# Optimization experiments

Hardware: AMD Instinct MI355X
Metric: run time of the kernel (lower is better)

The kernel has to match this reference:

```python
import jax, jax.numpy as jnp
import numpy as np

LN_EPS = 1e-5

def _ln(x, g, b):
    m = jnp.mean(x, -1, keepdims=True)
    v = jnp.mean((x - m) ** 2, -1, keepdims=True)
    return (x - m) / jnp.sqrt(v + LN_EPS) * g + b

def setup_inputs() -> dict:
    key = jax.random.key(0)
    N, E, D, F = 200000, 6400000, 128, 2048
    ks = iter(jax.random.split(key, 32))
    def rn(shape, sc):
        return jax.random.normal(next(ks), shape, jnp.float32) * sc
    inp = dict(
        x=rn((N, 3), 1.0),
        edge_index=jax.random.randint(next(ks), (2, E), 0, N),
        Win=rn((D, 3), 0.5), b_in=rn((D,), 0.02),
        Wv=rn((3, D, D), 0.08), bv=rn((3, D), 0.02),
        Wo=rn((3, D, D), 0.08), bo=rn((3, D), 0.02),
        W1=rn((3, F, D), 0.08), b1=rn((3, F), 0.02),
        W2=rn((3, D, F), 0.02), b2=rn((3, D), 0.02),
        ln1g=jnp.ones((3, D), jnp.float32), ln1b=jnp.zeros((3, D), jnp.float32),
        ln2g=jnp.ones((3, D), jnp.float32), ln2b=jnp.zeros((3, D), jnp.float32),
        Wd=rn((1, D), 0.08), bd=rn((1,), 0.02),
        Wg=rn((32, 1), 0.5), bg=rn((32,), 0.02),
        Wf=rn((1, 32), 0.2), bf=rn((1,), 0.02),
    )
    return inp

def reference(x, edge_index, Win, b_in, Wv, bv, Wo, bo, W1, b1, W2, b2,
              ln1g, ln1b, ln2g, ln2b, Wd, bd, Wg, bg, Wf, bf):
    N = x.shape[0]
    h = jax.nn.relu(x @ Win.T + b_in)  # [N, 128]
    # TransformerEncoder with seq_len == 1: softmax over a single key is 1,
    # so self-attention output == out_proj(value_proj(h)); post-norm layers.
    for i in range(3):
        attn = (h @ Wv[i].T + bv[i]) @ Wo[i].T + bo[i]
        h = _ln(h + attn, ln1g[i], ln1b[i])
        ff = jax.nn.relu(h @ W1[i].T + b1[i]) @ W2[i].T + b2[i]  # [N, 2048] intermediate
        h = _ln(h + ff, ln2g[i], ln2b[i])
    z = jax.nn.relu(h @ Wd.T + bd)  # [N, 1]
    # GCNConv(1, 32): add self-loops, symmetric D^-1/2 (A+I) D^-1/2 normalization
    self_idx = jnp.arange(N)
    row = jnp.concatenate([edge_index[0], self_idx])  # source
    col = jnp.concatenate([edge_index[1], self_idx])  # target
    xw = z @ Wg.T  # [N, 32]
    deg = jax.ops.segment_sum(jnp.ones_like(col, jnp.float32), col, num_segments=N)
    dis = jax.lax.rsqrt(jnp.maximum(deg, 1.0))
    norm = dis[row] * dis[col]  # [E + N]
    agg = jax.ops.segment_sum(xw[row] * norm[:, None], col, num_segments=N) + bg
    zr = jax.nn.relu(agg)  # [N, 32]
    return zr @ Wf.T + bf  # [N, 1]
```

## Files before the change

### kernel.cpp

```cpp
#include <hip/hip_runtime.h>
#include <hip/hip_bf16.h>
#include <stdint.h>

typedef __attribute__((ext_vector_type(8))) short short8;
typedef __attribute__((ext_vector_type(4))) float f32x4;

#define LN_EPS 1e-5f

__device__ __forceinline__ ushort f2bf(float f) {
  union { float f; uint32_t u; } v; v.f = f;
  uint32_t u = v.u;
  return (ushort)((u + 0x7FFFu + ((u >> 16) & 1u)) >> 16);
}
__device__ __forceinline__ float bf2f(ushort b) {
  union { uint32_t u; float f; } v; v.u = ((uint32_t)b) << 16;
  return v.f;
}
__device__ __forceinline__ uint32_t cvtpk(float lo, float hi) {
  uint32_t r;
  asm volatile("v_cvt_pk_bf16_f32 %0, %1, %2" : "=v"(r) : "v"(lo), "v"(hi));
  return r;
}


__global__ void conv_bf16_kernel(const float* __restrict__ src, ushort* __restrict__ dst, int n) {
  int i = blockIdx.x * 256 + threadIdx.x;
  if (i < n) dst[i] = f2bf(src[i]);
}

__global__ void zero_kernel(float* __restrict__ p, int n) {
  int i = blockIdx.x * 256 + threadIdx.x;
  if (i < n) p[i] = 0.f;
}

__global__ void embed_kernel(const float* __restrict__ x, const float* __restrict__ Win,
                             const float* __restrict__ b_in, float* __restrict__ h, int N) {
  int i = blockIdx.x * 256 + threadIdx.x;
  if (i >= N * 128) return;
  int n = i >> 7, d = i & 127;
  float v = Win[d*3+0]*x[n*3+0] + Win[d*3+1]*x[n*3+1] + Win[d*3+2]*x[n*3+2] + b_in[d];
  h[i] = fmaxf(v, 0.f);
}

__global__ void deg_kernel(const int* __restrict__ ei, float* __restrict__ degf, int E) {
  int i = blockIdx.x * 256 + threadIdx.x;
  int e0 = i * 4;
  if (e0 + 3 < E) {
    int4 c = *(const int4*)(ei + E + e0);
    atomicAdd(&degf[c.x], 1.0f); atomicAdd(&degf[c.y], 1.0f);
    atomicAdd(&degf[c.z], 1.0f); atomicAdd(&degf[c.w], 1.0f);
  } else {
    for (int e = e0; e < E; ++e) atomicAdd(&degf[ei[E + e]], 1.0f);
  }
}

__global__ void z_kernel(const float* __restrict__ h, const float* __restrict__ wd,
                         const float* __restrict__ bd, const float* __restrict__ degf,
                         float* __restrict__ u, int N) {
  int row = blockIdx.x * 4 + (threadIdx.x >> 6);
  int lane = threadIdx.x & 63;
  if (row >= N) return;
  const float* hr = h + (size_t)row * 128;
  float s = hr[lane] * wd[lane] + hr[64 + lane] * wd[64 + lane];
  #pragma unroll
  for (int o = 32; o >= 1; o >>= 1) s += __shfl_xor(s, o, 64);
  if (lane == 0) {
    float z = fmaxf(s + bd[0], 0.f);
    u[row] = z * rsqrtf(degf[row] + 1.0f);
  }
}

__global__ void scatter_kernel(const int* __restrict__ ei, const float* __restrict__ u,
                               float* __restrict__ t, int E) {
  int i = blockIdx.x * 256 + threadIdx.x;
  int e0 = i * 4;
  if (e0 + 3 < E) {
    int4 r = *(const int4*)(ei + e0);
    int4 c = *(const int4*)(ei + E + e0);
    atomicAdd(&t[c.x], u[r.x]); atomicAdd(&t[c.y], u[r.y]);
    atomicAdd(&t[c.z], u[r.z]); atomicAdd(&t[c.w], u[r.w]);
  } else {
    for (int e = e0; e < E; ++e) atomicAdd(&t[ei[E + e]], u[ei[e]]);
  }
}

__global__ void out_kernel(const float* __restrict__ degf, const float* __restrict__ u,
                           const float* __restrict__ t, const float* __restrict__ wg,
                           const float* __restrict__ bg, const float* __restrict__ wf,
                           const float* __restrict__ bfp, float* __restrict__ out, int N) {
  int n = blockIdx.x * 256 + threadIdx.x;
  if (n >= N) return;
  float dis = rsqrtf(degf[n] + 1.0f);
  float tf = dis * (t[n] + u[n]);
  float acc = bfp[0];
  #pragma unroll
  for (int j = 0; j < 32; ++j) acc += wf[j] * fmaxf(tf * wg[j] + bg[j], 0.f);
  out[n] = acc;
}


#define MFMA16(a, b, c) __builtin_amdgcn_mfma_f32_16x16x32_bf16(a, b, c, 0, 0, 0)

__global__ __launch_bounds__(512, 2) void layer_kernel(
    float* __restrict__ h,
    const ushort* __restrict__ Wv, const ushort* __restrict__ Wo,
    const ushort* __restrict__ W1, const ushort* __restrict__ W2,
    const float* __restrict__ bv, const float* __restrict__ bo,
    const float* __restrict__ b1, const float* __restrict__ b2,
    const float* __restrict__ g1, const float* __restrict__ be1,
    const float* __restrict__ g2, const float* __restrict__ be2,
    int N)
{
  __shared__ ushort hA[256 * 128];
  __shared__ ushort wbuf[2 * 16384];

  const int tid = threadIdx.x;
  const int lane = tid & 63;
  const int wave = tid >> 6;
  const int l15 = lane & 15;
  const int lg = lane >> 4;
  const int rowbase = blockIdx.x * 256;
  const int wrow = wave * 32;
  const int ssw = (l15 & 7) << 4;

  #pragma unroll
  for (int i = 0; i < 8; ++i) {
    int u = tid + i * 512;
    int row = u >> 4, k8 = u & 15;
    int g = rowbase + row;
    float4 f0 = make_float4(0.f,0.f,0.f,0.f), f1 = f0;
    if (g < N) {
      const float4* p = (const float4*)(h + (size_t)g * 128 + k8 * 8);
      f0 = p[0]; f1 = p[1];
    }
    short8 v;
    v[0]=(short)f2bf(f0.x); v[1]=(short)f2bf(f0.y); v[2]=(short)f2bf(f0.z); v[3]=(short)f2bf(f0.w);
    v[4]=(short)f2bf(f1.x); v[5]=(short)f2bf(f1.y); v[6]=(short)f2bf(f1.z); v[7]=(short)f2bf(f1.w);
    *(short8*)((char*)hA + ((row << 8) + ((k8 << 4) ^ ((row & 7) << 4)))) = v;
  }
  #pragma unroll
  for (int i = 0; i < 4; ++i) {
    int u = tid + i * 512;
    int row = u >> 4, k8 = u & 15;
    int off = (row << 8) + ((k8 << 4) ^ ((row & 7) << 4));
    *(short8*)((char*)wbuf + off)         = *(const short8*)(Wv + u * 8);
    *(short8*)((char*)wbuf + 32768 + off) = *(const short8*)(Wo + u * 8);
  }
  __syncthreads();

  short8 wr[4];
  #pragma unroll
  for (int i = 0; i < 4; ++i) {
    int c = tid + i * 512;
    wr[i] = (c < 1024) ? *(const short8*)(W1 + c * 8)
                       : *(const short8*)(W2 + (size_t)((c - 1024) >> 3) * 2048 + ((c - 1024) & 7) * 8);
  }

  f32x4 tC[2][8];
  #pragma unroll
  for (int rt = 0; rt < 2; ++rt)
    #pragma unroll
    for (int ct = 0; ct < 8; ++ct) tC[rt][ct] = (f32x4){0.f,0.f,0.f,0.f};
  __builtin_amdgcn_s_setprio(1);
  #pragma unroll
  for (int ks = 0; ks < 4; ++ks) {
    int asw = (ks * 64 + lg * 16) ^ ssw;
    short8 a0 = *(const short8*)((char*)hA + (((wrow + l15) << 8) + asw));
    short8 a1 = *(const short8*)((char*)hA + (((wrow + 16 + l15) << 8) + asw));
    #pragma unroll
    for (int ct = 0; ct < 8; ++ct) {
      short8 b = *(const short8*)((char*)wbuf + (((ct * 16 + l15) << 8) + asw));
      tC[0][ct] = MFMA16(a0, b, tC[0][ct]);
      tC[1][ct] = MFMA16(a1, b, tC[1][ct]);
    }
  }
  __builtin_amdgcn_s_setprio(0);
  #pragma unroll
  for (int ct = 0; ct < 8; ++ct) {
    int col = ct * 16 + l15;
    float bvv = bv[col];
    #pragma unroll
    for (int rt = 0; rt < 2; ++rt)
      #pragma unroll
      for (int j = 0; j < 4; ++j) {
        int lr = wrow + rt * 16 + lg * 4 + j;
        *(ushort*)((char*)hA + ((lr << 8) + ((col * 2) ^ ((lr & 7) << 4)))) =
            f2bf(tC[rt][ct][j] + bvv);
      }
  }
  __syncthreads();

  #pragma unroll
  for (int rt = 0; rt < 2; ++rt)
    #pragma unroll
    for (int ct = 0; ct < 8; ++ct) tC[rt][ct] = (f32x4){0.f,0.f,0.f,0.f};
  __builtin_amdgcn_s_setprio(1);
  #pragma unroll
  for (int ks = 0; ks < 4; ++ks) {
    int asw = (ks * 64 + lg * 16) ^ ssw;
    short8 a0 = *(const short8*)((char*)hA + (((wrow + l15) << 8) + asw));
    short8 a1 = *(const short8*)((char*)hA + (((wrow + 16 + l15) << 8) + asw));
    #pragma unroll
    for (int ct = 0; ct < 8; ++ct) {
      short8 b = *(const short8*)((char*)wbuf + 32768 + (((ct * 16 + l15) << 8) + asw));
      tC[0][ct] = MFMA16(a0, b, tC[0][ct]);
      tC[1][ct] = MFMA16(a1, b, tC[1][ct]);
    }
  }
  __builtin_amdgcn_s_setprio(0);

  float sum[2][4] = {{0,0,0,0},{0,0,0,0}};
  float sq[2][4]  = {{0,0,0,0},{0,0,0,0}};
  #pragma unroll
  for (int rt = 0; rt < 2; ++rt)
    #pragma unroll
    for (int ct = 0; ct < 8; ++ct) {
      float bov = bo[ct * 16 + l15];
      #pragma unroll
      for (int j = 0; j < 4; ++j) {
        int g = rowbase + wrow + rt * 16 + lg * 4 + j;
        float hv = (g < N) ? h[(size_t)g * 128 + ct * 16 + l15] : 0.f;
        float v = tC[rt][ct][j] + bov + hv;
        tC[rt][ct][j] = v;
        sum[rt][j] += v; sq[rt][j] += v * v;
      }
    }
  #pragma unroll
  for (int o = 1; o < 16; o <<= 1)
    #pragma unroll
    for (int rt = 0; rt < 2; ++rt)
      #pragma unroll
      for (int j = 0; j < 4; ++j) {
        sum[rt][j] += __shfl_xor(sum[rt][j], o, 64);
        sq[rt][j]  += __shfl_xor(sq[rt][j],  o, 64);
      }
  float mean[2][4], rstd[2][4];
  #pragma unroll
  for (int rt = 0; rt < 2; ++rt)
    #pragma unroll
    for (int j = 0; j < 4; ++j) {
      mean[rt][j] = sum[rt][j] * (1.f / 128.f);
      float var = sq[rt][j] * (1.f / 128.f) - mean[rt][j] * mean[rt][j];
      rstd[rt][j] = rsqrtf(var + LN_EPS);
    }
  #pragma unroll
  for (int ct = 0; ct < 8; ++ct) {
    int col = ct * 16 + l15;
    float g1v = g1[col], b1v = be1[col];
    #pragma unroll
    for (int rt = 0; rt < 2; ++rt)
      #pragma unroll
      for (int j = 0; j < 4; ++j) {
        int lr = wrow + rt * 16 + lg * 4 + j;
        float hh = (tC[rt][ct][j] - mean[rt][j]) * rstd[rt][j] * g1v + b1v;
        *(ushort*)((char*)hA + ((lr << 8) + ((col * 2) ^ ((lr & 7) << 4)))) = f2bf(hh);
      }
  }

  #pragma unroll
  for (int i = 0; i < 4; ++i) {
    int c = tid + i * 512;
    if (c < 1024) {
      int row = c >> 4, k8 = c & 15;
      *(short8*)((char*)wbuf + ((row << 8) + ((k8 << 4) ^ ((row & 7) << 4)))) = wr[i];
    } else {
      int cc = c - 1024;
      int row = cc >> 3, k8 = cc & 7;
      *(short8*)((char*)wbuf + 16384 + ((row << 7) + ((k8 << 4) ^ ((row & 7) << 4)))) = wr[i];
    }
  }
  {
    const ushort* W1c = W1 + 64 * 128;
    const ushort* W2c = W2 + 64;
    #pragma unroll
    for (int i = 0; i < 4; ++i) {
      int c = tid + i * 512;
      wr[i] = (c < 1024) ? *(const short8*)(W1c + c * 8)
                         : *(const short8*)(W2c + (size_t)((c - 1024) >> 3) * 2048 + ((c - 1024) & 7) * 8);
    }
  }
  __syncthreads();

  f32x4 acc[2][8];
  #pragma unroll
  for (int rt = 0; rt < 2; ++rt)
    #pragma unroll
    for (int ct = 0; ct < 8; ++ct) acc[rt][ct] = (f32x4){0.f,0.f,0.f,0.f};

  for (int ch = 0; ch < 32; ++ch) {
    const int base = (ch & 1) << 15;
    f32x4 uT[4][2];
    #pragma unroll
    for (int ft = 0; ft < 4; ++ft)
      #pragma unroll
      for (int rt = 0; rt < 2; ++rt) uT[ft][rt] = (f32x4){0.f,0.f,0.f,0.f};
    __builtin_amdgcn_s_setprio(1);
    #pragma unroll
    for (int ks = 0; ks < 4; ++ks) {
      int asw = (ks * 64 + lg * 16) ^ ssw;
      short8 bh[2];
      #pragma unroll
      for (int rt = 0; rt < 2; ++rt)
        bh[rt] = *(const short8*)((char*)hA + (((wrow + rt * 16 + l15) << 8) + asw));
      #pragma unroll
      for (int ft = 0; ft < 4; ++ft) {
        short8 aw = *(const short8*)((char*)wbuf + base + (((ft * 16 + l15) << 8) + asw));
        uT[ft][0] = MFMA16(aw, bh[0], uT[ft][0]);
        uT[ft][1] = MFMA16(aw, bh[1], uT[ft][1]);
      }
    }
    __builtin_amdgcn_s_setprio(0);
    #pragma unroll
    for (int ft = 0; ft < 4; ++ft) {
      float4 b4 = *(const float4*)(b1 + ch * 64 + ft * 16 + lg * 4);
      #pragma unroll
      for (int rt = 0; rt < 2; ++rt)
        #pragma unroll
        for (int j = 0; j < 4; ++j)
          uT[ft][rt][j] = fmaxf(uT[ft][rt][j] + ((const float*)&b4)[j], 0.f);
    }
    short8 fr[2][2];
    {
      const int s0 = l15 + ((lg & 1) << 5);
      const int s1 = s0 + 16;
      const bool hiq = (lg >= 2);
      #pragma unroll
      for (int ks2 = 0; ks2 < 2; ++ks2)
        #pragma unroll
        for (int rt = 0; rt < 2; ++rt) {
          uint32_t pA0 = cvtpk(uT[2*ks2][rt][0],   uT[2*ks2][rt][1]);
          uint32_t pA1 = cvtpk(uT[2*ks2][rt][2],   uT[2*ks2][rt][3]);
          uint32_t pB0 = cvtpk(uT[2*ks2+1][rt][0], uT[2*ks2+1][rt][1]);
          uint32_t pB1 = cvtpk(uT[2*ks2+1][rt][2], uT[2*ks2+1][rt][3]);
          uint32_t d0 = __shfl((int)pA0, s0, 64), d1 = __shfl((int)pA1, s0, 64);
          uint32_t d2 = __shfl((int)pA0, s1, 64), d3 = __shfl((int)pA1, s1, 64);
          uint32_t e0 = __shfl((int)pB0, s0, 64), e1 = __shfl((int)pB1, s0, 64);
          uint32_t e2 = __shfl((int)pB0, s1, 64), e3 = __shfl((int)pB1, s1, 64);
          union { uint32_t u[4]; short8 s; } f;
          f.u[0] = hiq ? e0 : d0; f.u[1] = hiq ? e1 : d1;
          f.u[2] = hiq ? e2 : d2; f.u[3] = hiq ? e3 : d3;
          fr[rt][ks2] = f.s;
        }
    }
    __builtin_amdgcn_s_setprio(1);
    #pragma unroll
    for (int ks2 = 0; ks2 < 2; ++ks2) {
      int asw2 = (ks2 * 64 + lg * 16) ^ ssw;
      #pragma unroll
      for (int ct = 0; ct < 8; ++ct) {
        short8 b = *(const short8*)((char*)wbuf + base + 16384 + (((ct * 16 + l15) << 7) + asw2));
        acc[0][ct] = MFMA16(fr[0][ks2], b, acc[0][ct]);
        acc[1][ct] = MFMA16(fr[1][ks2], b, acc[1][ct]);
      }
    }
    __builtin_amdgcn_s_setprio(0);

    if (ch < 31) {
      const int nbase = ((ch + 1) & 1) << 15;
      #pragma unroll
      for (int i = 0; i < 4; ++i) {
        int c = tid + i * 512;
        if (c < 1024) {
          int row = c >> 4, k8 = c & 15;
          *(short8*)((char*)wbuf + nbase + ((row << 8) + ((k8 << 4) ^ ((row & 7) << 4)))) = wr[i];
        } else {
          int cc = c - 1024;
          int row = cc >> 3, k8 = cc & 7;
          *(short8*)((char*)wbuf + nbase + 16384 + ((row << 7) + ((k8 << 4) ^ ((row & 7) << 4)))) = wr[i];
        }
      }
      if (ch < 30) {
        const ushort* W1c = W1 + (size_t)(ch + 2) * 64 * 128;
        const ushort* W2c = W2 + (ch + 2) * 64;
        #pragma unroll
        for (int i = 0; i < 4; ++i) {
          int c = tid + i * 512;
          wr[i] = (c < 1024) ? *(const short8*)(W1c + c * 8)
                             : *(const short8*)(W2c + (size_t)((c - 1024) >> 3) * 2048 + ((c - 1024) & 7) * 8);
        }
      }
      __syncthreads();
    }
  }

  #pragma unroll
  for (int rt = 0; rt < 2; ++rt)
    #pragma unroll
    for (int j = 0; j < 4; ++j) { sum[rt][j] = 0.f; sq[rt][j] = 0.f; }
  #pragma unroll
  for (int rt = 0; rt < 2; ++rt)
    #pragma unroll
    for (int ct = 0; ct < 8; ++ct) {
      int col = ct * 16 + l15;
      float b2v = b2[col];
      #pragma unroll
      for (int j = 0; j < 4; ++j) {
        int lr = wrow + rt * 16 + lg * 4 + j;
        float h1v = bf2f(*(const ushort*)((char*)hA + ((lr << 8) + ((col * 2) ^ ((lr & 7) << 4)))));
        float v = acc[rt][ct][j] + b2v + h1v;
        acc[rt][ct][j] = v;
        sum[rt][j] += v; sq[rt][j] += v * v;
      }
    }
  #pragma unroll
  for (int o = 1; o < 16; o <<= 1)
    #pragma unroll
    for (int rt = 0; rt < 2; ++rt)
      #pragma unroll
      for (int j = 0; j < 4; ++j) {
        sum[rt][j] += __shfl_xor(sum[rt][j], o, 64);
        sq[rt][j]  += __shfl_xor(sq[rt][j],  o, 64);
      }
  #pragma unroll
  for (int rt = 0; rt < 2; ++rt)
    #pragma unroll
    for (int j = 0; j < 4; ++j) {
      mean[rt][j] = sum[rt][j] * (1.f / 128.f);
      float var = sq[rt][j] * (1.f / 128.f) - mean[rt][j] * mean[rt][j];
      rstd[rt][j] = rsqrtf(var + LN_EPS);
    }
  #pragma unroll
  for (int rt = 0; rt < 2; ++rt)
    #pragma unroll
    for (int ct = 0; ct < 8; ++ct) {
      int col = ct * 16 + l15;
      float g2v = g2[col], b2lv = be2[col];
      #pragma unroll
      for (int j = 0; j < 4; ++j) {
        int g = rowbase + wrow + rt * 16 + lg * 4 + j;
        if (g < N)
          h[(size_t)g * 128 + col] = (acc[rt][ct][j] - mean[rt][j]) * rstd[rt][j] * g2v + b2lv;
      }
    }
}


extern "C" void kernel_launch(void* const* d_in, const int* in_sizes, int n_in,
                              void* d_out, int out_size, void* d_ws, size_t ws_size,
                              hipStream_t stream) {
  const float* x   = (const float*)d_in[0];
  const int*   ei  = (const int*)d_in[1];
  const float* Win = (const float*)d_in[2];
  const float* b_in= (const float*)d_in[3];
  const float* Wv  = (const float*)d_in[4];
  const float* bv  = (const float*)d_in[5];
  const float* Wo  = (const float*)d_in[6];
  const float* bo  = (const float*)d_in[7];
  const float* W1  = (const float*)d_in[8];
  const float* b1  = (const float*)d_in[9];
  const float* W2  = (const float*)d_in[10];
  const float* b2  = (const float*)d_in[11];
  const float* ln1g= (const float*)d_in[12];
  const float* ln1b= (const float*)d_in[13];
  const float* ln2g= (const float*)d_in[14];
  const float* ln2b= (const float*)d_in[15];
  const float* Wd  = (const float*)d_in[16];
  const float* bd  = (const float*)d_in[17];
  const float* Wg  = (const float*)d_in[18];
  const float* bg  = (const float*)d_in[19];
  const float* Wf  = (const float*)d_in[20];
  const float* bfp = (const float*)d_in[21];

  const int N = in_sizes[0] / 3;
  const int E = in_sizes[1] / 2;

  char* ws = (char*)d_ws;
  float* h = (float*)ws;                     size_t off = (size_t)N * 128 * 4;
  ushort* Wvb = (ushort*)(ws + off);         off += (size_t)3 * 16384 * 2;
  ushort* Wob = (ushort*)(ws + off);         off += (size_t)3 * 16384 * 2;
  ushort* W1b = (ushort*)(ws + off);         off += (size_t)3 * 262144 * 2;
  ushort* W2b = (ushort*)(ws + off);         off += (size_t)3 * 262144 * 2;
  float* degf = (float*)(ws + off);          off += (size_t)N * 4;
  float* tarr = (float*)(ws + off);          off += (size_t)N * 4;
  float* uarr = (float*)(ws + off);          off += (size_t)N * 4;

  conv_bf16_kernel<<<(3 * 16384 + 255) / 256, 256, 0, stream>>>(Wv, Wvb, 3 * 16384);
  conv_bf16_kernel<<<(3 * 16384 + 255) / 256, 256, 0, stream>>>(Wo, Wob, 3 * 16384);
  conv_bf16_kernel<<<(3 * 262144 + 255) / 256, 256, 0, stream>>>(W1, W1b, 3 * 262144);
  conv_bf16_kernel<<<(3 * 262144 + 255) / 256, 256, 0, stream>>>(W2, W2b, 3 * 262144);
  zero_kernel<<<(2 * N + 255) / 256, 256, 0, stream>>>(degf, 2 * N);

  embed_kernel<<<((size_t)N * 128 + 255) / 256, 256, 0, stream>>>(x, Win, b_in, h, N);
  deg_kernel<<<((E + 3) / 4 + 255) / 256, 256, 0, stream>>>(ei, degf, E);

  const int grid = (N + 255) / 256;
  for (int l = 0; l < 3; ++l) {
    layer_kernel<<<grid, 512, 0, stream>>>(
        h,
        Wvb + (size_t)l * 16384, Wob + (size_t)l * 16384,
        W1b + (size_t)l * 262144, W2b + (size_t)l * 262144,
        bv + l * 128, bo + l * 128, b1 + l * 2048, b2 + l * 128,
        ln1g + l * 128, ln1b + l * 128, ln2g + l * 128, ln2b + l * 128,
        N);
  }

  z_kernel<<<(N + 3) / 4, 256, 0, stream>>>(h, Wd, bd, degf, uarr, N);
  scatter_kernel<<<((E + 3) / 4 + 255) / 256, 256, 0, stream>>>(ei, uarr, tarr, E);
  out_kernel<<<(N + 255) / 256, 256, 0, stream>>>(degf, uarr, tarr, Wg, bg, Wf, bfp,
                                                  (float*)d_out, N);
}
```

Baseline: 2.145 ms.

## Shrink layer tiles to 192 rows, single weight buffer, new LDS fragment layout

Reworks the fused layer kernel to use 384-thread blocks over 192 rows with 3 blocks per CU. LDS shrinks by sharing one weight buffer between Wv and Wo, and the FFN moves to 32-wide chunks double-buffered in half the space. Weights are stored in an MFMA-fragment-ordered swizzled layout, and the h1 B-operands stay in registers across the FFN loop. The separate conversion, embedding and degree kernels are merged into one launch. In exchange it adds twice as many FFN chunk iterations and barriers, and per-thread register use may rise.

```diff
diff --git a/kernel.cpp b/kernel.cpp
--- a/kernel.cpp
+++ b/kernel.cpp
@@ -6,6 +6,7 @@
 typedef __attribute__((ext_vector_type(4))) float f32x4;
 
 #define LN_EPS 1e-5f
+#define MFMA16(a, b, c) __builtin_amdgcn_mfma_f32_16x16x32_bf16(a, b, c, 0, 0, 0)
 
 __device__ __forceinline__ ushort f2bf(float f) {
   union { float f; uint32_t u; } v; v.f = f;
@@ -23,36 +24,57 @@
 }
 
 
-__global__ void conv_bf16_kernel(const float* __restrict__ src, ushort* __restrict__ dst, int n) {
-  int i = blockIdx.x * 256 + threadIdx.x;
-  if (i < n) dst[i] = f2bf(src[i]);
-}
-
 __global__ void zero_kernel(float* __restrict__ p, int n) {
   int i = blockIdx.x * 256 + threadIdx.x;
   if (i < n) p[i] = 0.f;
 }
 
-__global__ void embed_kernel(const float* __restrict__ x, const float* __restrict__ Win,
-                             const float* __restrict__ b_in, float* __restrict__ h, int N) {
-  int i = blockIdx.x * 256 + threadIdx.x;
-  if (i >= N * 128) return;
-  int n = i >> 7, d = i & 127;
-  float v = Win[d*3+0]*x[n*3+0] + Win[d*3+1]*x[n*3+1] + Win[d*3+2]*x[n*3+2] + b_in[d];
-  h[i] = fmaxf(v, 0.f);
-}
-
-__global__ void deg_kernel(const int* __restrict__ ei, float* __restrict__ degf, int E) {
-  int i = blockIdx.x * 256 + threadIdx.x;
-  int e0 = i * 4;
-  if (e0 + 3 < E) {
-    int4 c = *(const int4*)(ei + E + e0);
-    atomicAdd(&degf[c.x], 1.0f); atomicAdd(&degf[c.y], 1.0f);
-    atomicAdd(&degf[c.z], 1.0f); atomicAdd(&degf[c.w], 1.0f);
-  } else {
-    for (int e = e0; e < E; ++e) atomicAdd(&degf[ei[E + e]], 1.0f);
-  }
-}
+__global__ void prep_kernel(
+    const float* __restrict__ x, const float* __restrict__ Win,
+    const float* __restrict__ b_in, float* __restrict__ h, int N,
+    const float* __restrict__ Wv, const float* __restrict__ Wo,
+    const float* __restrict__ W1, const float* __restrict__ W2,
+    ushort* __restrict__ Wvb, ushort* __restrict__ Wob,
+    ushort* __restrict__ W1b, ushort* __restrict__ W2b,
+    const int* __restrict__ ei, float* __restrict__ degf, int E,
+    int convBlocks, int embedBlocks)
+{
+  int bid = blockIdx.x;
+  if (bid < convBlocks) {
+    int i = bid * 256 + threadIdx.x;
+    if (i < 49152) { Wvb[i] = f2bf(Wv[i]); return; }
+    i -= 49152;
+    if (i < 49152) { Wob[i] = f2bf(Wo[i]); return; }
+    i -= 49152;
+    if (i < 786432) { W1b[i] = f2bf(W1[i]); return; }
+    i -= 786432;
+    if (i < 786432) W2b[i] = f2bf(W2[i]);
+    return;
+  }
+  bid -= convBlocks;
+  if (bid < embedBlocks) {
+    int i = bid * 256 + threadIdx.x;
+    if (i < N * 128) {
+      int n = i >> 7, d = i & 127;
+      float v = Win[d*3+0]*x[n*3+0] + Win[d*3+1]*x[n*3+1] + Win[d*3+2]*x[n*3+2] + b_in[d];
+      h[i] = fmaxf(v, 0.f);
+    }
+    return;
+  }
+  bid -= embedBlocks;
+  {
+    int i = bid * 256 + threadIdx.x;
+    int e0 = i * 4;
+    if (e0 + 3 < E) {
+      int4 c = *(const int4*)(ei + E + e0);
+      atomicAdd(&degf[c.x], 1.0f); atomicAdd(&degf[c.y], 1.0f);
+      atomicAdd(&degf[c.z], 1.0f); atomicAdd(&degf[c.w], 1.0f);
+    } else {
+      for (int e = e0; e < E; ++e) atomicAdd(&degf[ei[E + e]], 1.0f);
+    }
+  }
+}
+
 
 __global__ void z_kernel(const float* __restrict__ h, const float* __restrict__ wd,
                          const float* __restrict__ bd, const float* __restrict__ degf,
@@ -99,9 +121,7 @@
 }
 
 
-#define MFMA16(a, b, c) __builtin_amdgcn_mfma_f32_16x16x32_bf16(a, b, c, 0, 0, 0)
-
-__global__ __launch_bounds__(512, 2) void layer_kernel(
+__global__ __launch_bounds__(384, 3) void layer_kernel(
     float* __restrict__ h,
     const ushort* __restrict__ Wv, const ushort* __restrict__ Wo,
     const ushort* __restrict__ W1, const ushort* __restrict__ W2,
@@ -111,24 +131,25 @@
     const float* __restrict__ g2, const float* __restrict__ be2,
     int N)
 {
-  __shared__ ushort hA[256 * 128];
-  __shared__ ushort wbuf[2 * 16384];
+  __shared__ ushort hA[192 * 128];
+  __shared__ ushort wbuf[16384];
 
   const int tid = threadIdx.x;
   const int lane = tid & 63;
   const int wave = tid >> 6;
   const int l15 = lane & 15;
   const int lg = lane >> 4;
-  const int rowbase = blockIdx.x * 256;
+  const int rowbase = blockIdx.x * 192;
   const int wrow = wave * 32;
   const int ssw = (l15 & 7) << 4;
+  const int fswz = lg * 128 + ((l15 ^ (lg << 2)) << 3);
 
   #pragma unroll
   for (int i = 0; i < 8; ++i) {
-    int u = tid + i * 512;
+    int u = tid + i * 384;
     int row = u >> 4, k8 = u & 15;
     int g = rowbase + row;
-    float4 f0 = make_float4(0.f,0.f,0.f,0.f), f1 = f0;
+    float4 f0 = make_float4(0.f, 0.f, 0.f, 0.f), f1 = f0;
     if (g < N) {
       const float4* p = (const float4*)(h + (size_t)g * 128 + k8 * 8);
       f0 = p[0]; f1 = p[1];
@@ -139,28 +160,29 @@
     *(short8*)((char*)hA + ((row << 8) + ((k8 << 4) ^ ((row & 7) << 4)))) = v;
   }
   #pragma unroll
-  for (int i = 0; i < 4; ++i) {
-    int u = tid + i * 512;
-    int row = u >> 4, k8 = u & 15;
-    int off = (row << 8) + ((k8 << 4) ^ ((row & 7) << 4));
-    *(short8*)((char*)wbuf + off)         = *(const short8*)(Wv + u * 8);
-    *(short8*)((char*)wbuf + 32768 + off) = *(const short8*)(Wo + u * 8);
+  for (int i = 0; i < 6; ++i) {
+    int u = tid + i * 384;
+    if (u < 2048) {
+      short8 v = *(const short8*)(Wv + u * 8);
+      int col = u >> 4, k16 = u & 15;
+      int unit = (((col >> 4) << 2) + (k16 >> 2)) * 64 + (k16 & 3) * 16 + ((col & 15) ^ ((k16 & 3) << 2));
+      *(short8*)(wbuf + unit * 8) = v;
+    }
   }
   __syncthreads();
 
-  short8 wr[4];
-  #pragma unroll
-  for (int i = 0; i < 4; ++i) {
-    int c = tid + i * 512;
-    wr[i] = (c < 1024) ? *(const short8*)(W1 + c * 8)
-                       : *(const short8*)(W2 + (size_t)((c - 1024) >> 3) * 2048 + ((c - 1024) & 7) * 8);
+  short8 wo[6];
+  #pragma unroll
+  for (int i = 0; i < 6; ++i) {
+    int u = tid + i * 384;
+    if (u < 2048) wo[i] = *(const short8*)(Wo + u * 8);
   }
 
   f32x4 tC[2][8];
   #pragma unroll
   for (int rt = 0; rt < 2; ++rt)
     #pragma unroll
-    for (int ct = 0; ct < 8; ++ct) tC[rt][ct] = (f32x4){0.f,0.f,0.f,0.f};
+    for (int ct = 0; ct < 8; ++ct) tC[rt][ct] = (f32x4){0.f, 0.f, 0.f, 0.f};
   __builtin_amdgcn_s_setprio(1);
   #pragma unroll
   for (int ks = 0; ks < 4; ++ks) {
@@ -169,7 +191,7 @@
     short8 a1 = *(const short8*)((char*)hA + (((wrow + 16 + l15) << 8) + asw));
     #pragma unroll
     for (int ct = 0; ct < 8; ++ct) {
-      short8 b = *(const short8*)((char*)wbuf + (((ct * 16 + l15) << 8) + asw));
+      short8 b = *(const short8*)(wbuf + (ct * 4 + ks) * 512 + fswz);
       tC[0][ct] = MFMA16(a0, b, tC[0][ct]);
       tC[1][ct] = MFMA16(a1, b, tC[1][ct]);
     }
@@ -189,11 +211,32 @@
       }
   }
   __syncthreads();
-
-  #pragma unroll
-  for (int rt = 0; rt < 2; ++rt)
-    #pragma unroll
-    for (int ct = 0; ct < 8; ++ct) tC[rt][ct] = (f32x4){0.f,0.f,0.f,0.f};
+  #pragma unroll
+  for (int i = 0; i < 6; ++i) {
+    int u = tid + i * 384;
+    if (u < 2048) {
+      int col = u >> 4, k16 = u & 15;
+      int unit = (((col >> 4) << 2) + (k16 >> 2)) * 64 + (k16 & 3) * 16 + ((col & 15) ^ ((k16 & 3) << 2));
+      *(short8*)(wbuf + unit * 8) = wo[i];
+    }
+  }
+  __syncthreads();
+
+  short8 wr[3];
+  {
+    #pragma unroll
+    for (int i = 0; i < 3; ++i) {
+      int c = tid + i * 384;
+      if (i < 2 || c < 1024)
+        wr[i] = (c < 512) ? *(const short8*)(W1 + c * 8)
+                          : *(const short8*)(W2 + (size_t)((c - 512) >> 2) * 2048 + ((c - 512) & 3) * 8);
+    }
+  }
+
+  #pragma unroll
+  for (int rt = 0; rt < 2; ++rt)
+    #pragma unroll
+    for (int ct = 0; ct < 8; ++ct) tC[rt][ct] = (f32x4){0.f, 0.f, 0.f, 0.f};
   __builtin_amdgcn_s_setprio(1);
   #pragma unroll
   for (int ks = 0; ks < 4; ++ks) {
@@ -202,7 +245,7 @@
     short8 a1 = *(const short8*)((char*)hA + (((wrow + 16 + l15) << 8) + asw));
     #pragma unroll
     for (int ct = 0; ct < 8; ++ct) {
-      short8 b = *(const short8*)((char*)wbuf + 32768 + (((ct * 16 + l15) << 8) + asw));
+      short8 b = *(const short8*)(wbuf + (ct * 4 + ks) * 512 + fswz);
       tC[0][ct] = MFMA16(a0, b, tC[0][ct]);
       tC[1][ct] = MFMA16(a1, b, tC[1][ct]);
     }
@@ -257,26 +300,39 @@
       }
   }
 
-  #pragma unroll
-  for (int i = 0; i < 4; ++i) {
-    int c = tid + i * 512;
-    if (c < 1024) {
-      int row = c >> 4, k8 = c & 15;
-      *(short8*)((char*)wbuf + ((row << 8) + ((k8 << 4) ^ ((row & 7) << 4)))) = wr[i];
-    } else {
-      int cc = c - 1024;
-      int row = cc >> 3, k8 = cc & 7;
-      *(short8*)((char*)wbuf + 16384 + ((row << 7) + ((k8 << 4) ^ ((row & 7) << 4)))) = wr[i];
+  short8 h1B[2][4];
+  #pragma unroll
+  for (int rt = 0; rt < 2; ++rt)
+    #pragma unroll
+    for (int ks = 0; ks < 4; ++ks)
+      h1B[rt][ks] = *(const short8*)((char*)hA +
+          (((wrow + rt * 16 + l15) << 8) + ((ks * 64 + lg * 16) ^ ssw)));
+
+  __syncthreads();
+  #pragma unroll
+  for (int i = 0; i < 3; ++i) {
+    int c = tid + i * 384;
+    if (i < 2 || c < 1024) {
+      int unit;
+      if (c < 512) {
+        int f = c >> 4, k16 = c & 15;
+        unit = (((f >> 4) << 2) + (k16 >> 2)) * 64 + (k16 & 3) * 16 + ((f & 15) ^ ((k16 & 3) << 2));
+      } else {
+        int u2 = c - 512, d = u2 >> 2, fg = u2 & 3;
+        unit = 512 + (d >> 4) * 64 + fg * 16 + ((d & 15) ^ (fg << 2));
+      }
+      *(short8*)(wbuf + unit * 8) = wr[i];
     }
   }
   {
-    const ushort* W1c = W1 + 64 * 128;
-    const ushort* W2c = W2 + 64;
-    #pragma unroll
-    for (int i = 0; i < 4; ++i) {
-      int c = tid + i * 512;
-      wr[i] = (c < 1024) ? *(const short8*)(W1c + c * 8)
-                         : *(const short8*)(W2c + (size_t)((c - 1024) >> 3) * 2048 + ((c - 1024) & 7) * 8);
+    const ushort* W1c = W1 + 32 * 128;
+    const ushort* W2c = W2 + 32;
+    #pragma unroll
+    for (int i = 0; i < 3; ++i) {
+      int c = tid + i * 384;
+      if (i < 2 || c < 1024)
+        wr[i] = (c < 512) ? *(const short8*)(W1c + c * 8)
+                          : *(const short8*)(W2c + (size_t)((c - 512) >> 2) * 2048 + ((c - 512) & 3) * 8);
     }
   }
   __syncthreads();
@@ -285,98 +341,94 @@
   #pragma unroll
   for (int rt = 0; rt < 2; ++rt)
     #pragma unroll
-    for (int ct = 0; ct < 8; ++ct) acc[rt][ct] = (f32x4){0.f,0.f,0.f,0.f};
-
-  for (int ch = 0; ch < 32; ++ch) {
-    const int base = (ch & 1) << 15;
-    f32x4 uT[4][2];
-    #pragma unroll
-    for (int ft = 0; ft < 4; ++ft)
-      #pragma unroll
-      for (int rt = 0; rt < 2; ++rt) uT[ft][rt] = (f32x4){0.f,0.f,0.f,0.f};
+    for (int ct = 0; ct < 8; ++ct) acc[rt][ct] = (f32x4){0.f, 0.f, 0.f, 0.f};
+
+  for (int ch = 0; ch < 64; ++ch) {
+    const int b16 = (ch & 1) << 13;
+    f32x4 uT[2][2];
+    #pragma unroll
+    for (int ft = 0; ft < 2; ++ft)
+      #pragma unroll
+      for (int rt = 0; rt < 2; ++rt) uT[ft][rt] = (f32x4){0.f, 0.f, 0.f, 0.f};
     __builtin_amdgcn_s_setprio(1);
     #pragma unroll
     for (int ks = 0; ks < 4; ++ks) {
-      int asw = (ks * 64 + lg * 16) ^ ssw;
-      short8 bh[2];
-      #pragma unroll
-      for (int rt = 0; rt < 2; ++rt)
-        bh[rt] = *(const short8*)((char*)hA + (((wrow + rt * 16 + l15) << 8) + asw));
-      #pragma unroll
-      for (int ft = 0; ft < 4; ++ft) {
-        short8 aw = *(const short8*)((char*)wbuf + base + (((ft * 16 + l15) << 8) + asw));
-        uT[ft][0] = MFMA16(aw, bh[0], uT[ft][0]);
-        uT[ft][1] = MFMA16(aw, bh[1], uT[ft][1]);
-      }
+      short8 aw0 = *(const short8*)(wbuf + b16 + (0 * 4 + ks) * 512 + fswz);
+      short8 aw1 = *(const short8*)(wbuf + b16 + (1 * 4 + ks) * 512 + fswz);
+      uT[0][0] = MFMA16(aw0, h1B[0][ks], uT[0][0]);
+      uT[0][1] = MFMA16(aw0, h1B[1][ks], uT[0][1]);
+      uT[1][0] = MFMA16(aw1, h1B[0][ks], uT[1][0]);
+      uT[1][1] = MFMA16(aw1, h1B[1][ks], uT[1][1]);
     }
     __builtin_amdgcn_s_setprio(0);
     #pragma unroll
-    for (int ft = 0; ft < 4; ++ft) {
-      float4 b4 = *(const float4*)(b1 + ch * 64 + ft * 16 + lg * 4);
-      #pragma unroll
-      for (int rt = 0; rt < 2; ++rt)
-        #pragma unroll
-        for (int j = 0; j < 4; ++j)
-          uT[ft][rt][j] = fmaxf(uT[ft][rt][j] + ((const float*)&b4)[j], 0.f);
-    }
-    short8 fr[2][2];
+    for (int ft = 0; ft < 2; ++ft) {
+      float4 b4 = *(const float4*)(b1 + ch * 32 + ft * 16 + lg * 4);
+      #pragma unroll
+      for (int rt = 0; rt < 2; ++rt) {
+        uT[ft][rt][0] = fmaxf(uT[ft][rt][0] + b4.x, 0.f);
+        uT[ft][rt][1] = fmaxf(uT[ft][rt][1] + b4.y, 0.f);
+        uT[ft][rt][2] = fmaxf(uT[ft][rt][2] + b4.z, 0.f);
+        uT[ft][rt][3] = fmaxf(uT[ft][rt][3] + b4.w, 0.f);
+      }
+    }
+    short8 fr[2];
     {
       const int s0 = l15 + ((lg & 1) << 5);
       const int s1 = s0 + 16;
       const bool hiq = (lg >= 2);
       #pragma unroll
-      for (int ks2 = 0; ks2 < 2; ++ks2)
+      for (int rt = 0; rt < 2; ++rt) {
+        uint32_t pA0 = cvtpk(uT[0][rt][0], uT[0][rt][1]);
+        uint32_t pA1 = cvtpk(uT[0][rt][2], uT[0][rt][3]);
+        uint32_t pB0 = cvtpk(uT[1][rt][0], uT[1][rt][1]);
+        uint32_t pB1 = cvtpk(uT[1][rt][2], uT[1][rt][3]);
+        uint32_t d0 = __shfl((int)pA0, s0, 64), d1 = __shfl((int)pA1, s0, 64);
+        uint32_t d2 = __shfl((int)pA0, s1, 64), d3 = __shfl((int)pA1, s1, 64);
+        uint32_t e0 = __shfl((int)pB0, s0, 64), e1 = __shfl((int)pB1, s0, 64);
+        uint32_t e2 = __shfl((int)pB0, s1, 64), e3 = __shfl((int)pB1, s1, 64);
+        union { uint32_t u[4]; short8 s; } f;
+        f.u[0] = hiq ? e0 : d0; f.u[1] = hiq ? e1 : d1;
+        f.u[2] = hiq ? e2 : d2; f.u[3] = hiq ? e3 : d3;
+        fr[rt] = f.s;
+      }
+    }
+    __builtin_amdgcn_s_setprio(1);
+    #pragma unroll
+    for (int ct = 0; ct < 8; ++ct) {
+      short8 b = *(const short8*)(wbuf + b16 + 4096 + ct * 512 + fswz);
+      acc[0][ct] = MFMA16(fr[0], b, acc[0][ct]);
+      acc[1][ct] = MFMA16(fr[1], b, acc[1][ct]);
+    }
+    __builtin_amdgcn_s_setprio(0);
+
+    if (ch < 63) {
+      __syncthreads();
+      const int nb16 = ((ch + 1) & 1) << 13;
+      #pragma unroll
+      for (int i = 0; i < 3; ++i) {
+        int c = tid + i * 384;
+        if (i < 2 || c < 1024) {
+          int unit;
+          if (c < 512) {
+            int f = c >> 4, k16 = c & 15;
+            unit = (((f >> 4) << 2) + (k16 >> 2)) * 64 + (k16 & 3) * 16 + ((f & 15) ^ ((k16 & 3) << 2));
+          } else {
+            int u2 = c - 512, d = u2 >> 2, fg = u2 & 3;
+            unit = 512 + (d >> 4) * 64 + fg * 16 + ((d & 15) ^ (fg << 2));
+          }
+          *(short8*)(wbuf + nb16 + unit * 8) = wr[i];
+        }
+      }
+      if (ch < 62) {
+        const ushort* W1c = W1 + (size_t)(ch + 2) * 32 * 128;
+        const ushort* W2c = W2 + (ch + 2) * 32;
         #pragma unroll
-        for (int rt = 0; rt < 2; ++rt) {
-          uint32_t pA0 = cvtpk(uT[2*ks2][rt][0],   uT[2*ks2][rt][1]);
-          uint32_t pA1 = cvtpk(uT[2*ks2][rt][2],   uT[2*ks2][rt][3]);
-          uint32_t pB0 = cvtpk(uT[2*ks2+1][rt][0], uT[2*ks2+1][rt][1]);
-          uint32_t pB1 = cvtpk(uT[2*ks2+1][rt][2], uT[2*ks2+1][rt][3]);
-          uint32_t d0 = __shfl((int)pA0, s0, 64), d1 = __shfl((int)pA1, s0, 64);
-          uint32_t d2 = __shfl((int)pA0, s1, 64), d3 = __shfl((int)pA1, s1, 64);
-          uint32_t e0 = __shfl((int)pB0, s0, 64), e1 = __shfl((int)pB1, s0, 64);
-          uint32_t e2 = __shfl((int)pB0, s1, 64), e3 = __shfl((int)pB1, s1, 64);
-          union { uint32_t u[4]; short8 s; } f;
-          f.u[0] = hiq ? e0 : d0; f.u[1] = hiq ? e1 : d1;
-          f.u[2] = hiq ? e2 : d2; f.u[3] = hiq ? e3 : d3;
-          fr[rt][ks2] = f.s;
-        }
-    }
-    __builtin_amdgcn_s_setprio(1);
-    #pragma unroll
-    for (int ks2 = 0; ks2 < 2; ++ks2) {
-      int asw2 = (ks2 * 64 + lg * 16) ^ ssw;
-      #pragma unroll
-      for (int ct = 0; ct < 8; ++ct) {
-        short8 b = *(const short8*)((char*)wbuf + base + 16384 + (((ct * 16 + l15) << 7) + asw2));
-        acc[0][ct] = MFMA16(fr[0][ks2], b, acc[0][ct]);
-        acc[1][ct] = MFMA16(fr[1][ks2], b, acc[1][ct]);
-      }
-    }
-    __builtin_amdgcn_s_setprio(0);
-
-    if (ch < 31) {
-      const int nbase = ((ch + 1) & 1) << 15;
-      #pragma unroll
-      for (int i = 0; i < 4; ++i) {
-        int c = tid + i * 512;
-        if (c < 1024) {
-          int row = c >> 4, k8 = c & 15;
-          *(short8*)((char*)wbuf + nbase + ((row << 8) + ((k8 << 4) ^ ((row & 7) << 4)))) = wr[i];
-        } else {
-          int cc = c - 1024;
-          int row = cc >> 3, k8 = cc & 7;
-          *(short8*)((char*)wbuf + nbase + 16384 + ((row << 7) + ((k8 << 4) ^ ((row & 7) << 4)))) = wr[i];
-        }
-      }
-      if (ch < 30) {
-        const ushort* W1c = W1 + (size_t)(ch + 2) * 64 * 128;
-        const ushort* W2c = W2 + (ch + 2) * 64;
-        #pragma unroll
-        for (int i = 0; i < 4; ++i) {
-          int c = tid + i * 512;
-          wr[i] = (c < 1024) ? *(const short8*)(W1c + c * 8)
-                             : *(const short8*)(W2c + (size_t)((c - 1024) >> 3) * 2048 + ((c - 1024) & 7) * 8);
+        for (int i = 0; i < 3; ++i) {
+          int c = tid + i * 384;
+          if (i < 2 || c < 1024)
+            wr[i] = (c < 512) ? *(const short8*)(W1c + c * 8)
+                              : *(const short8*)(W2c + (size_t)((c - 512) >> 2) * 2048 + ((c - 512) & 3) * 8);
         }
       }
       __syncthreads();
@@ -474,18 +526,18 @@
   float* tarr = (float*)(ws + off);          off += (size_t)N * 4;
   float* uarr = (float*)(ws + off);          off += (size_t)N * 4;
 
-  conv_bf16_kernel<<<(3 * 16384 + 255) / 256, 256, 0, stream>>>(Wv, Wvb, 3 * 16384);
-  conv_bf16_kernel<<<(3 * 16384 + 255) / 256, 256, 0, stream>>>(Wo, Wob, 3 * 16384);
-  conv_bf16_kernel<<<(3 * 262144 + 255) / 256, 256, 0, stream>>>(W1, W1b, 3 * 262144);
-  conv_bf16_kernel<<<(3 * 262144 + 255) / 256, 256, 0, stream>>>(W2, W2b, 3 * 262144);
   zero_kernel<<<(2 * N + 255) / 256, 256, 0, stream>>>(degf, 2 * N);
 
-  embed_kernel<<<((size_t)N * 128 + 255) / 256, 256, 0, stream>>>(x, Win, b_in, h, N);
-  deg_kernel<<<((E + 3) / 4 + 255) / 256, 256, 0, stream>>>(ei, degf, E);
-
-  const int grid = (N + 255) / 256;
+  const int convBlocks = 1671168 / 256;
+  const int embedBlocks = (N * 128 + 255) / 256;
+  const int degBlocks = ((E + 3) / 4 + 255) / 256;
+  prep_kernel<<<convBlocks + embedBlocks + degBlocks, 256, 0, stream>>>(
+      x, Win, b_in, h, N, Wv, Wo, W1, W2, Wvb, Wob, W1b, W2b,
+      ei, degf, E, convBlocks, embedBlocks);
+
+  const int grid = (N + 191) / 192;
   for (int l = 0; l < 3; ++l) {
-    layer_kernel<<<grid, 512, 0, stream>>>(
+    layer_kernel<<<grid, 384, 0, stream>>>(
         h,
         Wvb + (size_t)l * 16384, Wob + (size_t)l * 16384,
         W1b + (size_t)l * 262144, W2b + (size_t)l * 262144,
```

Result: slower. 3.177 ms (+48.1%).
